# Kernel tuning notes

Hardware: AMD Instinct MI355X
Metric: run time of the kernel (lower is better)

## Reference

```python
import jax, jax.numpy as jnp
import numpy as np

ACTION_IDS = jnp.array([7, 8, 9])
PREF_IDS = jnp.array([10, 11])
SPECIAL_IDS = jnp.array([0, 1, 2])  # <PAD>, <BOS>, <EOS>
NEG = -1e9


def setup_inputs() -> dict:
    key = jax.random.key(0)
    k1, k2 = jax.random.split(key)
    input_ids = jax.random.randint(k1, (1, 8192), 0, 16)
    emb_weight = jax.random.normal(k2, (16, 64), dtype=jnp.float32) * 0.02
    return {"input_ids": input_ids, "emb_weight": emb_weight}


def reference(input_ids, emb_weight):
    ids = input_ids[0]                      # [L]
    L = ids.shape[0]
    V = emb_weight.shape[0]

    # hidden states: plain embedding lookup
    h = emb_weight[input_ids]               # [1, L, 64]

    # ---- rule-based logits ----
    tok = jnp.arange(V)
    is_pref_tok = jnp.isin(tok, PREF_IDS)
    is_special_tok = jnp.isin(tok, SPECIAL_IDS)
    # row when previous token is an action: only pref tokens get 5.0
    row_action = jnp.where(is_pref_tok, 5.0, NEG)
    # row otherwise: 1.0 for non-special tokens, then pref tokens overwritten to -5.0
    row_other = jnp.where(is_pref_tok, -5.0, jnp.where(is_special_tok, NEG, 1.0))

    prev_is_action = jnp.isin(ids[:-1], ACTION_IDS)           # [L-1]
    next_logits = jnp.where(prev_is_action[:, None], row_action[None, :], row_other[None, :])  # [L-1, V]
    logits = jnp.concatenate([jnp.full((1, V), NEG, dtype=jnp.float32),
                              next_logits.astype(jnp.float32)], axis=0)[None]  # [1, L, V]

    # ---- rule-based attention ----
    i = jnp.arange(L)
    is_pref = jnp.isin(ids, PREF_IDS)                          # token i is a preference word
    prev_action = jnp.concatenate([jnp.zeros((1,), bool), jnp.isin(ids[:-1], ACTION_IDS)])
    cond = is_pref & (i > 0) & prev_action                     # rows with focused attention

    each = 0.2 / (L - 1)
    # focused row: 0.8 on column i-1, 0.2/(L-1) everywhere else
    special = jnp.where(i[None, :] == (i - 1)[:, None], 0.8, each)  # [L, L]
    attn = jnp.where(cond[:, None], special, 1.0 / L)[None, None]   # [1, 1, L, L]
    attn = attn.astype(jnp.float32)

    return logits, attn, h
```

## Files before the change

### kernel.cpp

```cpp
#include <hip/hip_runtime.h>
#include <hip/hip_bf16.h>


#define VOCAB 16
#define DIM 64
#define NEGV -1e9f

typedef float f32x4 __attribute__((ext_vector_type(4)));

__global__ __launch_bounds__(256) void rulelm_fused(
    const int* __restrict__ ids,
    const float* __restrict__ emb,
    float* __restrict__ logits,
    float* __restrict__ attn,
    float* __restrict__ h,
    int L)
{
    const int i   = blockIdx.x;
    const int tid = threadIdx.x;

    const int id  = ids[i];
    const int idp = (i > 0) ? ids[i - 1] : -1;

    const bool prev_action = (i > 0) && (idp >= 7 && idp <= 9);
    const bool is_pref     = (id == 10) || (id == 11);
    const bool cond        = is_pref && prev_action;

    if (tid < VOCAB) {
        float val;
        const bool tok_pref = (tid == 10) || (tid == 11);
        if (i == 0) {
            val = NEGV;
        } else if (prev_action) {
            val = tok_pref ? 5.0f : NEGV;
        } else {
            val = tok_pref ? -5.0f : ((tid <= 2) ? NEGV : 1.0f);
        }
        logits[(size_t)i * VOCAB + tid] = val;
    } else if (tid >= 64 && tid < 80) {
        const int q = tid - 64;
        ((float4*)(h + (size_t)i * DIM))[q] =
            ((const float4*)(emb + (size_t)id * DIM))[q];
    }

    const float each = 0.2f / (float)(L - 1);
    const float base = cond ? each : (1.0f / (float)L);
    const f32x4 fill = {base, base, base, base};

    f32x4* __restrict__ arow = (f32x4*)(attn + (size_t)i * (size_t)L);
    const int nvec  = L >> 2;
    const int iters = nvec >> 8;

    if ((L & 1023) == 0) {
        if (!cond) {
            f32x4* p = arow + tid;
#pragma unroll 8
            for (int t = 0; t < iters; ++t) {
                __builtin_nontemporal_store(fill, p);
                p += 256;
            }
        } else {
            const int ks = (i - 1) >> 2;
            const int kl = (i - 1) & 3;
            f32x4* p = arow + tid;
            int k = tid;
#pragma unroll 8
            for (int t = 0; t < iters; ++t) {
                f32x4 w = fill;
                if (k == ks) w[kl] = 0.8f;
                __builtin_nontemporal_store(w, p);
                p += 256;
                k += 256;
            }
        }
    } else {
        const int special = cond ? (i - 1) : -1;
        for (int k = tid; k < nvec; k += 256) {
            f32x4 w = fill;
            const int c0 = k << 2;
            if (special >= c0 && special < c0 + 4) {
                w[special - c0] = 0.8f;
            }
            __builtin_nontemporal_store(w, arow + k);
        }
    }
}

extern "C" void kernel_launch(void* const* d_in, const int* in_sizes, int n_in,
                              void* d_out, int out_size, void* d_ws, size_t ws_size,
                              hipStream_t stream)
{
    const int*   ids = (const int*)d_in[0];
    const float* emb = (const float*)d_in[1];
    const int L = in_sizes[0];

    float* out    = (float*)d_out;
    float* logits = out;
    float* attn   = out + (size_t)L * VOCAB;
    float* h      = attn + (size_t)L * (size_t)L;

    rulelm_fused<<<L, 256, 0, stream>>>(ids, emb, logits, attn, h, L);
}
```

Before: 54.63 us.

## Process four attention rows per block and use regular stores instead of nontemporal

Adds a kernel variant where each block writes four consecutive rows of logits, hidden states and the attention matrix, reusing the loaded ids for the previous-token check. It launches a quarter as many blocks and replaces nontemporal stores with ordinary cached stores. The fallback single-row kernel is simplified to a generic loop with a scalar tail for any L. The trade-off is less block-level parallelism per row and possible cache pollution from regular stores on a write-bound 256MB output.

```diff
diff --git a/kernel.cpp b/kernel.cpp
--- a/kernel.cpp
+++ b/kernel.cpp
@@ -5,10 +5,85 @@
 #define VOCAB 16
 #define DIM 64
 #define NEGV -1e9f
+#define ROWS 4
 
 typedef float f32x4 __attribute__((ext_vector_type(4)));
 
-__global__ __launch_bounds__(256) void rulelm_fused(
+__global__ __launch_bounds__(256) void rulelm_fused4(
+    const int* __restrict__ ids,
+    const float* __restrict__ emb,
+    float* __restrict__ logits,
+    float* __restrict__ attn,
+    float* __restrict__ h,
+    int L)
+{
+    const int i0  = blockIdx.x * ROWS;
+    const int tid = threadIdx.x;
+
+    int idv[ROWS];
+#pragma unroll
+    for (int r = 0; r < ROWS; ++r) idv[r] = ids[i0 + r];
+    const int idm1 = (i0 > 0) ? ids[i0 - 1] : -1;
+
+#pragma unroll
+    for (int r = 0; r < ROWS; ++r) {
+        const int i   = i0 + r;
+        const int id  = idv[r];
+        const int idp = (r == 0) ? idm1 : idv[r - 1];
+
+        const bool prev_action = (i > 0) && (idp >= 7 && idp <= 9);
+        const bool is_pref     = (id == 10) || (id == 11);
+        const bool cond        = is_pref && prev_action;
+
+        if (tid < VOCAB) {
+            float val;
+            const bool tok_pref = (tid == 10) || (tid == 11);
+            if (i == 0) {
+                val = NEGV;
+            } else if (prev_action) {
+                val = tok_pref ? 5.0f : NEGV;
+            } else {
+                val = tok_pref ? -5.0f : ((tid <= 2) ? NEGV : 1.0f);
+            }
+            logits[(size_t)i * VOCAB + tid] = val;
+        } else if (tid >= 64 && tid < 80) {
+            const int q = tid - 64;
+            ((float4*)(h + (size_t)i * DIM))[q] =
+                ((const float4*)(emb + (size_t)id * DIM))[q];
+        }
+
+        const float each = 0.2f / (float)(L - 1);
+        const float base = cond ? each : (1.0f / (float)L);
+        const f32x4 fill = {base, base, base, base};
+
+        f32x4* __restrict__ arow = (f32x4*)(attn + (size_t)i * (size_t)L);
+        const int iters = (L >> 2) >> 8;
+
+        if (!cond) {
+            f32x4* p = arow + tid;
+#pragma unroll 8
+            for (int t = 0; t < iters; ++t) {
+                *p = fill;
+                p += 256;
+            }
+        } else {
+            const int ks = (i - 1) >> 2;
+            const int kl = (i - 1) & 3;
+            f32x4* p = arow + tid;
+            int k = tid;
+#pragma unroll 8
+            for (int t = 0; t < iters; ++t) {
+                f32x4 w = fill;
+                if (k == ks) w[kl] = 0.8f;
+                *p = w;
+                p += 256;
+                k += 256;
+            }
+        }
+    }
+}
+
+__global__ __launch_bounds__(256) void rulelm_fused1(
     const int* __restrict__ ids,
     const float* __restrict__ emb,
     float* __restrict__ logits,
@@ -45,44 +120,16 @@
 
     const float each = 0.2f / (float)(L - 1);
     const float base = cond ? each : (1.0f / (float)L);
-    const f32x4 fill = {base, base, base, base};
+    const int special = cond ? (i - 1) : -1;
 
-    f32x4* __restrict__ arow = (f32x4*)(attn + (size_t)i * (size_t)L);
-    const int nvec  = L >> 2;
-    const int iters = nvec >> 8;
-
-    if ((L & 1023) == 0) {
-        if (!cond) {
-            f32x4* p = arow + tid;
-#pragma unroll 8
-            for (int t = 0; t < iters; ++t) {
-                __builtin_nontemporal_store(fill, p);
-                p += 256;
-            }
-        } else {
-            const int ks = (i - 1) >> 2;
-            const int kl = (i - 1) & 3;
-            f32x4* p = arow + tid;
-            int k = tid;
-#pragma unroll 8
-            for (int t = 0; t < iters; ++t) {
-                f32x4 w = fill;
-                if (k == ks) w[kl] = 0.8f;
-                __builtin_nontemporal_store(w, p);
-                p += 256;
-                k += 256;
-            }
-        }
-    } else {
-        const int special = cond ? (i - 1) : -1;
-        for (int k = tid; k < nvec; k += 256) {
-            f32x4 w = fill;
-            const int c0 = k << 2;
-            if (special >= c0 && special < c0 + 4) {
-                w[special - c0] = 0.8f;
-            }
-            __builtin_nontemporal_store(w, arow + k);
-        }
+    float* row = attn + (size_t)i * (size_t)L;
+    for (int c = tid * 4; c < L; c += 1024) {
+        f32x4 w = {base, base, base, base};
+        if (special >= c && special < c + 4) w[special - c] = 0.8f;
+        *(f32x4*)(row + c) = w;
+    }
+    for (int c = (L & ~3) + tid; c < L; c += 256) {
+        row[c] = (c == special) ? 0.8f : base;
     }
 }
 
@@ -99,5 +146,9 @@
     float* attn   = out + (size_t)L * VOCAB;
     float* h      = attn + (size_t)L * (size_t)L;
 
-    rulelm_fused<<<L, 256, 0, stream>>>(ids, emb, logits, attn, h, L);
+    if ((L % (ROWS * 1024)) == 0) {
+        rulelm_fused4<<<L / ROWS, 256, 0, stream>>>(ids, emb, logits, attn, h, L);
+    } else {
+        rulelm_fused1<<<L, 256, 0, stream>>>(ids, emb, logits, attn, h, L);
+    }
 }
```

After: 48.10 us. -12.0%, faster.
